# Kernel tuning notes

Hardware: AMD Instinct MI355X
Metric: run time of the kernel (lower is better)

Reference implementation:

```python
import jax, jax.numpy as jnp
import numpy as np

DIM = 512
NUM_HEADS = 8
HEAD_DIM = DIM // NUM_HEADS        # 64
L_HEADS = 4                        # int(8 * 0.5)
H_HEADS = NUM_HEADS - L_HEADS      # 4
L_DIM = L_HEADS * HEAD_DIM         # 256
H_DIM = H_HEADS * HEAD_DIM         # 256
WS = 2                             # window_size
SCALE = HEAD_DIM ** -0.5
SEQ_LEN = 1024


def setup_inputs() -> dict:
    key = jax.random.key(0)
    ks = jax.random.split(key, 13)
    B, N, C = 16, 1024, DIM
    def w(k, shape, fan_in):
        return (jax.random.normal(k, shape, jnp.float32) / np.sqrt(fan_in)).astype(jnp.float32)
    return {
        "x": jax.random.normal(ks[0], (B, N, C), jnp.float32),
        "pos_emb": jax.random.normal(ks[1], (1, SEQ_LEN, C), jnp.float32) * 0.02,
        "l_q_w": w(ks[2], (C, L_DIM), C),
        "l_kv_w": w(ks[3], (C, 2 * L_DIM), C),
        "l_proj_w": w(ks[4], (L_DIM, L_DIM), L_DIM),
        "l_proj_b": jax.random.normal(ks[5], (L_DIM,), jnp.float32) * 0.01,
        "h_qkv_w": w(ks[6], (C, 3 * H_DIM), C),
        "h_proj_w": w(ks[7], (H_DIM, H_DIM), H_DIM),
        "h_proj_b": jax.random.normal(ks[8], (H_DIM,), jnp.float32) * 0.01,
        "in_proj_w": w(ks[9], (C, 3 * C), C),
        "in_proj_b": jax.random.normal(ks[10], (3 * C,), jnp.float32) * 0.01,
        "out_proj_w": w(ks[11], (C, C), C),
        "out_proj_b": jax.random.normal(ks[12], (C,), jnp.float32) * 0.01,
        "H": 32,
        "W": 32,
    }


def _hifi(xg, h_qkv_w, h_proj_w, h_proj_b, H, W):
    B, _, _, C = xg.shape
    hg, wg = H // WS, W // WS
    G, T = hg * wg, WS * WS
    # [B, hg, WS, wg, WS, C] -> [B, G, T, C] (window partition)
    xw = xg.reshape(B, hg, WS, wg, WS, C).transpose(0, 1, 3, 2, 4, 5).reshape(B, G, T, C)
    qkv = (xw @ h_qkv_w).reshape(B, G, T, 3, H_HEADS, HEAD_DIM)
    q = qkv[:, :, :, 0].transpose(0, 1, 3, 2, 4)  # [B,G,h,T,d]
    k = qkv[:, :, :, 1].transpose(0, 1, 3, 2, 4)
    v = qkv[:, :, :, 2].transpose(0, 1, 3, 2, 4)
    attn = jax.nn.softmax(jnp.einsum("bghtd,bghsd->bghts", q, k) * SCALE, axis=-1)
    o = jnp.einsum("bghts,bghsd->bghtd", attn, v)
    # window un-partition: [B,G,h,T,d] -> [B,H,W,h_dim]
    o = o.transpose(0, 1, 3, 2, 4).reshape(B, hg, wg, WS, WS, H_DIM)
    o = o.transpose(0, 1, 3, 2, 4, 5).reshape(B, H, W, H_DIM)
    return o @ h_proj_w + h_proj_b


def _lofi(xg, l_q_w, l_kv_w, l_proj_w, l_proj_b, H, W):
    B, _, _, C = xg.shape
    N = H * W
    q = (xg @ l_q_w).reshape(B, N, L_HEADS, HEAD_DIM)
    kv = (xg @ l_kv_w).reshape(B, N, 2, L_HEADS, HEAD_DIM)
    k, v = kv[:, :, 0], kv[:, :, 1]
    attn = jax.nn.softmax(jnp.einsum("bnhd,bmhd->bhnm", q, k) * SCALE, axis=-1)
    o = jnp.einsum("bhnm,bmhd->bnhd", attn, v).reshape(B, H, W, L_DIM)
    return o @ l_proj_w + l_proj_b


def _mha(y, in_proj_w, in_proj_b, out_proj_w, out_proj_b):
    B, N, C = y.shape
    qkv = y @ in_proj_w + in_proj_b
    q, k, v = jnp.split(qkv, 3, axis=-1)
    q = q.reshape(B, N, NUM_HEADS, HEAD_DIM)
    k = k.reshape(B, N, NUM_HEADS, HEAD_DIM)
    v = v.reshape(B, N, NUM_HEADS, HEAD_DIM)
    attn = jax.nn.softmax(jnp.einsum("bnhd,bmhd->bhnm", q, k) * SCALE, axis=-1)
    o = jnp.einsum("bhnm,bmhd->bnhd", attn, v).reshape(B, N, C)
    return o @ out_proj_w + out_proj_b


def reference(x, pos_emb, l_q_w, l_kv_w, l_proj_w, l_proj_b,
              h_qkv_w, h_proj_w, h_proj_b,
              in_proj_w, in_proj_b, out_proj_w, out_proj_b, H, W):
    B, N, C = x.shape
    x = x + pos_emb[:, :N, :]
    xg = x.reshape(B, H, W, C)
    hifi_out = _hifi(xg, h_qkv_w, h_proj_w, h_proj_b, H, W)
    lofi_out = _lofi(xg, l_q_w, l_kv_w, l_proj_w, l_proj_b, H, W)
    y = jnp.concatenate([hifi_out, lofi_out], axis=-1).reshape(B, N, C)
    return _mha(y, in_proj_w, in_proj_b, out_proj_w, out_proj_b)
```

## Files before the change

### kernel.cpp

```cpp
#include <hip/hip_runtime.h>

typedef unsigned short ushort_t;
typedef short bf16x8 __attribute__((ext_vector_type(8)));
typedef float f32x4 __attribute__((ext_vector_type(4)));
typedef float f32x16 __attribute__((ext_vector_type(16)));

#define DEV __device__ __forceinline__

DEV ushort_t f2bf(float f) {
  return (ushort_t)((__float_as_uint(f) + 0x8000u) >> 16);
}
DEV unsigned pk_bf16(float lo, float hi) {
  unsigned a = __float_as_uint(lo) + 0x8000u;
  unsigned b = __float_as_uint(hi) + 0x8000u;
  return __builtin_amdgcn_perm(b, a, 0x07060302);
}
DEV float bf2f(ushort_t h) {
  union { unsigned int u; float f; } v; v.u = ((unsigned int)h) << 16;
  return v.f;
}
DEV f32x4 mfma16(bf16x8 a, bf16x8 b, f32x4 c) {
  return __builtin_amdgcn_mfma_f32_16x16x32_bf16(a, b, c, 0, 0, 0);
}
DEV f32x16 mfma32(bf16x8 a, bf16x8 b, f32x16 c) {
  return __builtin_amdgcn_mfma_f32_32x32x16_bf16(a, b, c, 0, 0, 0);
}
DEV void pl32swap(unsigned &a, unsigned &b) {
  asm("v_permlane32_swap_b32 %0, %1" : "+v"(a), "+v"(b));
}
typedef __attribute__((address_space(3))) void lds_void;
typedef const __attribute__((address_space(1))) void glb_void;
DEV void gl_lds16(const void* g, void* l) {
  __builtin_amdgcn_global_load_lds((glb_void*)g, (lds_void*)l, 16, 0, 0);
}

__global__ __launch_bounds__(256)
void gemm_bt(const ushort_t* __restrict__ A, int lda,
             const ushort_t* __restrict__ BT,
             const float* __restrict__ bias,
             ushort_t* __restrict__ Cb, float* __restrict__ Cf,
             int ldc, int coff, int K, float scv, int sc_lo, int sc_hi)
{
  __shared__ __align__(16) ushort_t As[128 * 32];
  __shared__ __align__(16) ushort_t Bs[128 * 32];
  const int tid  = threadIdx.x;
  const int wave = tid >> 6, lane = tid & 63;
  const int quad = lane >> 4, r16 = lane & 15;
  const int m0 = blockIdx.x * 128, n0 = blockIdx.y * 128;
  const int wm = (wave >> 1) * 64, wn = (wave & 1) * 64;

  f32x4 acc[4][4];
#pragma unroll
  for (int i = 0; i < 4; ++i)
#pragma unroll
    for (int j = 0; j < 4; ++j) acc[i][j] = (f32x4){0.f, 0.f, 0.f, 0.f};

  for (int kc = 0; kc < K; kc += 32) {
#pragma unroll
    for (int p = 0; p < 4; ++p) {
      int wp = p * 4 + wave;
      int lc = ((wp & 7) << 6) + lane;
      int row = lc >> 2, e8 = (lc & 3) * 8;
      if (wp < 8) gl_lds16(&A[(size_t)(m0 + row) * lda + kc + e8], &As[lc * 8]);
      else        gl_lds16(&BT[(size_t)(n0 + row) * K  + kc + e8], &Bs[lc * 8]);
    }
    __syncthreads();
    bf16x8 af[4], bfr[4];
#pragma unroll
    for (int i = 0; i < 4; ++i) {
      af[i]  = *(const bf16x8*)&As[(wm + i * 16 + r16) * 32 + quad * 8];
      bfr[i] = *(const bf16x8*)&Bs[(wn + i * 16 + r16) * 32 + quad * 8];
    }
#pragma unroll
    for (int mi = 0; mi < 4; ++mi)
#pragma unroll
      for (int ni = 0; ni < 4; ++ni)
        acc[mi][ni] = mfma16(af[mi], bfr[ni], acc[mi][ni]);
    __syncthreads();
  }

#pragma unroll
  for (int mi = 0; mi < 4; ++mi) {
#pragma unroll
    for (int ni = 0; ni < 4; ++ni) {
      int col = n0 + wn + ni * 16 + r16;
      float bv = bias ? bias[col] : 0.f;
      float s = (col >= sc_lo && col < sc_hi) ? scv : 1.0f;
#pragma unroll
      for (int r = 0; r < 4; ++r) {
        int row = m0 + wm + mi * 16 + quad * 4 + r;
        float v = (acc[mi][ni][r] + bv) * s;
        if (Cf) Cf[(size_t)row * ldc + coff + col] = v;
        else    Cb[(size_t)row * ldc + coff + col] = f2bf(v);
      }
    }
  }
}

template<int QG>
__global__ __launch_bounds__(256, 2)
void flash_attn9(const ushort_t* __restrict__ Q, int qs, int q_ch,
                 const ushort_t* __restrict__ Kg, int ks, int k_ch,
                 const ushort_t* __restrict__ vT,
                 ushort_t* __restrict__ O, int os, int o_ch,
                 int N)
{
  __shared__ __align__(16) ushort_t Ks[2][64 * 64];
  __shared__ __align__(16) ushort_t Vs[2][64 * 64];

  const int H = gridDim.y;
  const int tid = threadIdx.x, wave = tid >> 6, lane = tid & 63;
  const int c = lane & 31, hh = lane >> 5;

  const int nwg = gridDim.x * H * gridDim.z;
  const int lin = blockIdx.x + gridDim.x * (blockIdx.y + H * blockIdx.z);
  const int logical = (lin & 7) * (nwg >> 3) + (lin >> 3);
  const int QBS = 8 / QG;
  const int qb = logical & (QBS - 1);
  const int t8 = logical / QBS;
  const int b = (H == 8) ? (t8 >> 3) : (t8 >> 2);
  const int h = t8 - b * H;
  const int q0 = qb * (128 * QG) + wave * (32 * QG);

  bf16x8 qf[QG][4];
#pragma unroll
  for (int qg = 0; qg < QG; ++qg) {
    const ushort_t* qp =
        Q + ((size_t)b * N + q0 + qg * 32 + c) * qs + q_ch + h * 64 + hh * 8;
#pragma unroll
    for (int s = 0; s < 4; ++s) qf[qg][s] = *(const bf16x8*)&qp[s * 16];
  }
  const ushort_t* kbase = Kg + ((size_t)b * N) * ks + k_ch + h * 64;
  const ushort_t* vbase = vT + ((size_t)(b * H + h) * 64) * N;

  f32x16 oacc[QG][2];
#pragma unroll
  for (int qg = 0; qg < QG; ++qg)
#pragma unroll
    for (int i = 0; i < 16; ++i) { oacc[qg][0][i] = 0.f; oacc[qg][1][i] = 0.f; }
  float l_acc[QG];
#pragma unroll
  for (int qg = 0; qg < QG; ++qg) l_acc[qg] = 0.f;

  auto stage = [&](int s0, int buf) {
#pragma unroll
    for (int p = 0; p < 4; ++p) {
      int wp = p * 4 + wave;
      int lc = ((wp & 7) << 6) + lane;
      int row = lc >> 3, cc = lc & 7;
      int e8 = ((cc ^ (row & 7)) * 8);
      if (wp < 8) gl_lds16(kbase + (size_t)(s0 + row) * ks + e8, &Ks[buf][lc * 8]);
      else        gl_lds16(vbase + (size_t)row * N + s0 + e8,    &Vs[buf][lc * 8]);
    }
  };

  stage(0, 0);
  const int NT = N >> 6;
  for (int it = 0; it < NT; ++it) {
    const int cur = it & 1;
    __syncthreads();
    if (it + 1 < NT) stage((it + 1) << 6, cur ^ 1);

    bf16x8 Bf[QG][4];
#pragma unroll
    for (int kb = 0; kb < 2; ++kb) {
      const int krow = kb * 32 + c;
      const ushort_t* kr = &Ks[cur][krow * 64];
      bf16x8 kf[4];
#pragma unroll
      for (int s = 0; s < 4; ++s)
        kf[s] = *(const bf16x8*)&kr[(((s << 1) + hh) ^ (krow & 7)) * 8];

#pragma unroll
      for (int qg = 0; qg < QG; ++qg) {
        f32x16 z;
#pragma unroll
        for (int i = 0; i < 16; ++i) z[i] = 0.f;
#pragma unroll
        for (int s = 0; s < 4; ++s) z = mfma32(kf[s], qf[qg][s], z);
        float ts = 0.f;
        unsigned W[8];
#pragma unroll
        for (int t = 0; t < 8; ++t) {
          float p0 = __builtin_amdgcn_exp2f(z[2 * t]);
          float p1 = __builtin_amdgcn_exp2f(z[2 * t + 1]);
          ts += p0 + p1;
          W[t] = pk_bf16(p0, p1);
        }
        l_acc[qg] += ts;
        union U8 { bf16x8 f; unsigned u[4]; } f0, f1;
        unsigned a0 = W[0], b0 = W[2]; pl32swap(a0, b0);
        unsigned a1 = W[1], b1 = W[3]; pl32swap(a1, b1);
        f0.u[0] = a0; f0.u[1] = a1; f0.u[2] = b0; f0.u[3] = b1;
        unsigned a2 = W[4], b2 = W[6]; pl32swap(a2, b2);
        unsigned a3 = W[5], b3 = W[7]; pl32swap(a3, b3);
        f1.u[0] = a2; f1.u[1] = a3; f1.u[2] = b2; f1.u[3] = b3;
        Bf[qg][kb * 2]     = f0.f;
        Bf[qg][kb * 2 + 1] = f1.f;
      }
    }

#pragma unroll
    for (int db = 0; db < 2; ++db) {
      const int vrow = db * 32 + c;
      const ushort_t* vr = &Vs[cur][vrow * 64];
      bf16x8 vf[4];
#pragma unroll
      for (int s = 0; s < 4; ++s)
        vf[s] = *(const bf16x8*)&vr[(((s << 1) + hh) ^ (vrow & 7)) * 8];
#pragma unroll
      for (int qg = 0; qg < QG; ++qg)
#pragma unroll
        for (int s = 0; s < 4; ++s)
          oacc[qg][db] = mfma32(vf[s], Bf[qg][s], oacc[qg][db]);
    }
  }

#pragma unroll
  for (int qg = 0; qg < QG; ++qg) {
    float l = l_acc[qg] + __shfl_xor(l_acc[qg], 32);
    float inv = 1.f / l;
    ushort_t* op = O + ((size_t)b * N + q0 + qg * 32 + c) * os + o_ch + h * 64;
#pragma unroll
    for (int db = 0; db < 2; ++db) {
#pragma unroll
      for (int g = 0; g < 4; ++g) {
        uint2 pkv;
        pkv.x = pk_bf16(oacc[qg][db][4 * g + 0] * inv, oacc[qg][db][4 * g + 1] * inv);
        pkv.y = pk_bf16(oacc[qg][db][4 * g + 2] * inv, oacc[qg][db][4 * g + 3] * inv);
        *(uint2*)&op[db * 32 + g * 8 + hh * 4] = pkv;
      }
    }
  }
}

__global__ __launch_bounds__(256)
void transpose_v(const ushort_t* __restrict__ in, int ld, int ch,
                 ushort_t* __restrict__ out, int N, int H)
{
  __shared__ __align__(16) ushort_t T[64][72];
  const int s0 = blockIdx.x * 64, h = blockIdx.y, b = blockIdx.z;
  const int tid = threadIdx.x;
#pragma unroll
  for (int p = 0; p < 2; ++p) {
    int c = p * 256 + tid;
    int sr = c >> 3, d0 = (c & 7) * 8;
    *(uint4*)&T[sr][d0] =
        *(const uint4*)&in[((size_t)b * N + s0 + sr) * ld + ch + h * 64 + d0];
  }
  __syncthreads();
  const int d = tid >> 2, sp = (tid & 3) * 16;
  union { uint4 v; ushort_t u[8]; } A, B;
#pragma unroll
  for (int j = 0; j < 8; ++j) { A.u[j] = T[sp + j][d]; B.u[j] = T[sp + 8 + j][d]; }
  ushort_t* op = out + ((size_t)(b * H + h) * 64 + d) * N + s0 + sp;
  *(uint4*)&op[0] = A.v;
  *(uint4*)&op[8] = B.v;
}

__global__ __launch_bounds__(256)
void hifi_win(const ushort_t* __restrict__ qkv, int ld, ushort_t* __restrict__ out)
{
  const int bg = blockIdx.x;
  const int b = bg >> 8, g = bg & 255;
  const int head = threadIdx.x >> 6, lane = threadIdx.x & 63;
  const int gh = g >> 4, gw = g & 15;

  int n[4];
  float q[4], k[4], v[4];
#pragma unroll
  for (int t = 0; t < 4; ++t) {
    n[t] = (gh * 2 + (t >> 1)) * 32 + gw * 2 + (t & 1);
    size_t base = ((size_t)b * 1024 + n[t]) * ld + head * 64 + lane;
    q[t] = bf2f(qkv[base]);
    k[t] = bf2f(qkv[base + 256]);
    v[t] = bf2f(qkv[base + 512]);
  }
  float sc[4][4];
#pragma unroll
  for (int t = 0; t < 4; ++t)
#pragma unroll
    for (int s = 0; s < 4; ++s) {
      float p = q[t] * k[s];
#pragma unroll
      for (int off = 32; off >= 1; off >>= 1) p += __shfl_xor(p, off);
      sc[t][s] = p * 0.125f;
    }
#pragma unroll
  for (int t = 0; t < 4; ++t) {
    float m = fmaxf(fmaxf(sc[t][0], sc[t][1]), fmaxf(sc[t][2], sc[t][3]));
    float p0 = __expf(sc[t][0] - m), p1 = __expf(sc[t][1] - m);
    float p2 = __expf(sc[t][2] - m), p3 = __expf(sc[t][3] - m);
    float sum = p0 + p1 + p2 + p3;
    float o = (p0 * v[0] + p1 * v[1] + p2 * v[2] + p3 * v[3]) / sum;
    out[((size_t)b * 1024 + n[t]) * 512 + head * 64 + lane] = f2bf(o);
  }
}

struct WEnt { const float* W; ushort_t* WT; int K; int N; };
struct WArgs { WEnt e[7]; };

__global__ __launch_bounds__(256)
void w_prep(WArgs a)
{
  WEnt w = a.e[blockIdx.z];
  if ((int)blockIdx.x >= (w.K >> 6) || (int)blockIdx.y >= (w.N >> 6)) return;
  __shared__ float T[64][65];
  const int k0 = blockIdx.x * 64, n0 = blockIdx.y * 64;
  const int tid = threadIdx.x;
#pragma unroll
  for (int p = 0; p < 4; ++p) {
    int c = p * 256 + tid;
    int kr = c >> 4, f4 = (c & 15) * 4;
    float4 v = *(const float4*)&w.W[(size_t)(k0 + kr) * w.N + n0 + f4];
    T[f4 + 0][kr] = v.x; T[f4 + 1][kr] = v.y;
    T[f4 + 2][kr] = v.z; T[f4 + 3][kr] = v.w;
  }
  __syncthreads();
  const int nl = tid >> 2, kp = (tid & 3) * 16;
  union { uint4 v; ushort_t u[8]; } A, B;
#pragma unroll
  for (int j = 0; j < 8; ++j) {
    A.u[j] = f2bf(T[nl][kp + j]);
    B.u[j] = f2bf(T[nl][kp + 8 + j]);
  }
  ushort_t* op = w.WT + (size_t)(n0 + nl) * w.K + k0 + kp;
  *(uint4*)&op[0] = A.v;
  *(uint4*)&op[8] = B.v;
}

__global__ void add_pos(const float* __restrict__ x, const float* __restrict__ pos,
                        ushort_t* __restrict__ xpe)
{
  int idx = blockIdx.x * 256 + threadIdx.x;
  int e = idx * 4;
  float4 xv = *(const float4*)&x[e];
  float4 pv = *(const float4*)&pos[e & (512 * 1024 - 1)];
  uint2 pk;
  pk.x = pk_bf16(xv.x + pv.x, xv.y + pv.y);
  pk.y = pk_bf16(xv.z + pv.z, xv.w + pv.w);
  *(uint2*)&xpe[e] = pk;
}

extern "C" void kernel_launch(void* const* d_in, const int* in_sizes, int n_in,
                              void* d_out, int out_size, void* d_ws, size_t ws_size,
                              hipStream_t stream)
{
  const float* x         = (const float*)d_in[0];
  const float* pos       = (const float*)d_in[1];
  const float* l_q_w     = (const float*)d_in[2];
  const float* l_kv_w    = (const float*)d_in[3];
  const float* l_proj_w  = (const float*)d_in[4];
  const float* l_proj_b  = (const float*)d_in[5];
  const float* h_qkv_w   = (const float*)d_in[6];
  const float* h_proj_w  = (const float*)d_in[7];
  const float* h_proj_b  = (const float*)d_in[8];
  const float* in_proj_w = (const float*)d_in[9];
  const float* in_proj_b = (const float*)d_in[10];
  const float* out_proj_w= (const float*)d_in[11];
  const float* out_proj_b= (const float*)d_in[12];
  float* out = (float*)d_out;

  const float QSCALE = 0.125f * 1.44269504f;

  char* ws = (char*)d_ws;
  ushort_t* xpe = (ushort_t*)(ws);
  ushort_t* y   = (ushort_t*)(ws + (size_t)16777216);
  ushort_t* F   = (ushort_t*)(ws + (size_t)33554432);
  ushort_t* rB  = (ushort_t*)(ws + (size_t)83886080);
  ushort_t* wb  = (ushort_t*)(ws + (size_t)100663296);

  ushort_t* F_T      = wb;
  ushort_t* h_projT  = wb + 786432;
  ushort_t* l_projT  = wb + 851968;
  ushort_t* in_projT = wb + 917504;
  ushort_t* out_projT= wb + 1703936;

  const int M = 16384;
  ushort_t* vT_lo = xpe;
  ushort_t* vT_m  = rB;

  WArgs wa;
  wa.e[0] = {h_qkv_w,   F_T,                 512, 768};
  wa.e[1] = {l_q_w,     F_T + 768 * 512,     512, 256};
  wa.e[2] = {l_kv_w,    F_T + 1024 * 512,    512, 512};
  wa.e[3] = {h_proj_w,  h_projT,             256, 256};
  wa.e[4] = {l_proj_w,  l_projT,             256, 256};
  wa.e[5] = {in_proj_w, in_projT,            512, 1536};
  wa.e[6] = {out_proj_w,out_projT,           512, 512};
  w_prep<<<dim3(8, 24, 7), dim3(256), 0, stream>>>(wa);

  add_pos<<<dim3(8192), dim3(256), 0, stream>>>(x, pos, xpe);

  gemm_bt<<<dim3(M / 128, 12), dim3(256), 0, stream>>>(
      xpe, 512, F_T, nullptr, F, nullptr, 1536, 0, 512, QSCALE, 768, 1024);
  hifi_win<<<dim3(4096), dim3(256), 0, stream>>>(F, 1536, rB);
  transpose_v<<<dim3(16, 4, 16), dim3(256), 0, stream>>>(
      F, 1536, 1280, vT_lo, 1024, 4);
  flash_attn9<1><<<dim3(8, 4, 16), dim3(256), 0, stream>>>(
      F, 1536, 768, F, 1536, 1024, vT_lo, rB, 512, 256, 1024);
  gemm_bt<<<dim3(M / 128, 2), dim3(256), 0, stream>>>(
      rB, 512, h_projT, h_proj_b, y, nullptr, 512, 0, 256, 1.0f, 0, 0);
  gemm_bt<<<dim3(M / 128, 2), dim3(256), 0, stream>>>(
      rB + 256, 512, l_projT, l_proj_b, y, nullptr, 512, 256, 256, 1.0f, 0, 0);
  gemm_bt<<<dim3(M / 128, 12), dim3(256), 0, stream>>>(
      y, 512, in_projT, in_proj_b, F, nullptr, 1536, 0, 512, QSCALE, 0, 512);
  transpose_v<<<dim3(16, 8, 16), dim3(256), 0, stream>>>(
      F, 1536, 1024, vT_m, 1024, 8);
  flash_attn9<2><<<dim3(4, 8, 16), dim3(256), 0, stream>>>(
      F, 1536, 0, F, 1536, 512, vT_m, xpe, 512, 0, 1024);
  gemm_bt<<<dim3(M / 128, 4), dim3(256), 0, stream>>>(
      xpe, 512, out_projT, out_proj_b, nullptr, out, 512, 0, 512, 1.0f, 0, 0);
}
```

Before: 335.4 us.

## Merge hifi/lofi projection GEMMs, remap GEMM tiles across XCDs, use hardware bf16 pack

```diff
diff --git a/kernel.cpp b/kernel.cpp
--- a/kernel.cpp
+++ b/kernel.cpp
@@ -14,6 +14,11 @@
   unsigned a = __float_as_uint(lo) + 0x8000u;
   unsigned b = __float_as_uint(hi) + 0x8000u;
   return __builtin_amdgcn_perm(b, a, 0x07060302);
+}
+DEV unsigned cvtpk_bf16(float lo, float hi) {
+  unsigned r;
+  asm("v_cvt_pk_bf16_f32 %0, %1, %2" : "=v"(r) : "v"(lo), "v"(hi));
+  return r;
 }
 DEV float bf2f(ushort_t h) {
   union { unsigned int u; float f; } v; v.u = ((unsigned int)h) << 16;
@@ -46,7 +51,12 @@
   const int tid  = threadIdx.x;
   const int wave = tid >> 6, lane = tid & 63;
   const int quad = lane >> 4, r16 = lane & 15;
-  const int m0 = blockIdx.x * 128, n0 = blockIdx.y * 128;
+  const int nwg = gridDim.x * gridDim.y;
+  const int lin = blockIdx.x + gridDim.x * blockIdx.y;
+  const int logical = (lin & 7) * (nwg >> 3) + (lin >> 3);
+  const int nbn = gridDim.y;
+  const int mb = logical / nbn, nb = logical - mb * nbn;
+  const int m0 = mb * 128, n0 = nb * 128;
   const int wm = (wave >> 1) * 64, wn = (wave & 1) * 64;
 
   f32x4 acc[4][4];
@@ -92,6 +102,72 @@
         float v = (acc[mi][ni][r] + bv) * s;
         if (Cf) Cf[(size_t)row * ldc + coff + col] = v;
         else    Cb[(size_t)row * ldc + coff + col] = f2bf(v);
+      }
+    }
+  }
+}
+
+__global__ __launch_bounds__(256)
+void gemm_proj(const ushort_t* __restrict__ rB,
+               const ushort_t* __restrict__ hT, const ushort_t* __restrict__ lT,
+               const float* __restrict__ hb, const float* __restrict__ lb,
+               ushort_t* __restrict__ y)
+{
+  __shared__ __align__(16) ushort_t As[128 * 32];
+  __shared__ __align__(16) ushort_t Bs[128 * 32];
+  const int tid  = threadIdx.x;
+  const int wave = tid >> 6, lane = tid & 63;
+  const int quad = lane >> 4, r16 = lane & 15;
+  const int lin = blockIdx.x + 128 * blockIdx.y;
+  const int logical = (lin & 7) * 64 + (lin >> 3);
+  const int nidx = logical & 3, m0 = (logical >> 2) * 128;
+  const int sel = nidx >> 1, n0 = (nidx & 1) * 128;
+  const ushort_t* A  = rB + sel * 256;
+  const ushort_t* BT = sel ? lT : hT;
+  const float* bias  = sel ? lb : hb;
+  const int coff = sel * 256;
+  const int wm = (wave >> 1) * 64, wn = (wave & 1) * 64;
+
+  f32x4 acc[4][4];
+#pragma unroll
+  for (int i = 0; i < 4; ++i)
+#pragma unroll
+    for (int j = 0; j < 4; ++j) acc[i][j] = (f32x4){0.f, 0.f, 0.f, 0.f};
+
+  for (int kc = 0; kc < 256; kc += 32) {
+#pragma unroll
+    for (int p = 0; p < 4; ++p) {
+      int wp = p * 4 + wave;
+      int lc = ((wp & 7) << 6) + lane;
+      int row = lc >> 2, e8 = (lc & 3) * 8;
+      if (wp < 8) gl_lds16(&A[(size_t)(m0 + row) * 512 + kc + e8], &As[lc * 8]);
+      else        gl_lds16(&BT[(size_t)(n0 + row) * 256 + kc + e8], &Bs[lc * 8]);
+    }
+    __syncthreads();
+    bf16x8 af[4], bfr[4];
+#pragma unroll
+    for (int i = 0; i < 4; ++i) {
+      af[i]  = *(const bf16x8*)&As[(wm + i * 16 + r16) * 32 + quad * 8];
+      bfr[i] = *(const bf16x8*)&Bs[(wn + i * 16 + r16) * 32 + quad * 8];
+    }
+#pragma unroll
+    for (int mi = 0; mi < 4; ++mi)
+#pragma unroll
+      for (int ni = 0; ni < 4; ++ni)
+        acc[mi][ni] = mfma16(af[mi], bfr[ni], acc[mi][ni]);
+    __syncthreads();
+  }
+
+#pragma unroll
+  for (int mi = 0; mi < 4; ++mi) {
+#pragma unroll
+    for (int ni = 0; ni < 4; ++ni) {
+      int col = n0 + wn + ni * 16 + r16;
+      float bv = bias[col];
+#pragma unroll
+      for (int r = 0; r < 4; ++r) {
+        int row = m0 + wm + mi * 16 + quad * 4 + r;
+        y[(size_t)row * 512 + coff + col] = f2bf(acc[mi][ni][r] + bv);
       }
     }
   }
@@ -185,7 +261,7 @@
           float p0 = __builtin_amdgcn_exp2f(z[2 * t]);
           float p1 = __builtin_amdgcn_exp2f(z[2 * t + 1]);
           ts += p0 + p1;
-          W[t] = pk_bf16(p0, p1);
+          W[t] = cvtpk_bf16(p0, p1);
         }
         l_acc[qg] += ts;
         union U8 { bf16x8 f; unsigned u[4]; } f0, f1;
@@ -226,8 +302,8 @@
 #pragma unroll
       for (int g = 0; g < 4; ++g) {
         uint2 pkv;
-        pkv.x = pk_bf16(oacc[qg][db][4 * g + 0] * inv, oacc[qg][db][4 * g + 1] * inv);
-        pkv.y = pk_bf16(oacc[qg][db][4 * g + 2] * inv, oacc[qg][db][4 * g + 3] * inv);
+        pkv.x = cvtpk_bf16(oacc[qg][db][4 * g + 0] * inv, oacc[qg][db][4 * g + 1] * inv);
+        pkv.y = cvtpk_bf16(oacc[qg][db][4 * g + 2] * inv, oacc[qg][db][4 * g + 3] * inv);
         *(uint2*)&op[db * 32 + g * 8 + hh * 4] = pkv;
       }
     }
@@ -399,10 +475,8 @@
       F, 1536, 1280, vT_lo, 1024, 4);
   flash_attn9<1><<<dim3(8, 4, 16), dim3(256), 0, stream>>>(
       F, 1536, 768, F, 1536, 1024, vT_lo, rB, 512, 256, 1024);
-  gemm_bt<<<dim3(M / 128, 2), dim3(256), 0, stream>>>(
-      rB, 512, h_projT, h_proj_b, y, nullptr, 512, 0, 256, 1.0f, 0, 0);
-  gemm_bt<<<dim3(M / 128, 2), dim3(256), 0, stream>>>(
-      rB + 256, 512, l_projT, l_proj_b, y, nullptr, 512, 256, 256, 1.0f, 0, 0);
+  gemm_proj<<<dim3(128, 4), dim3(256), 0, stream>>>(
+      rB, h_projT, l_projT, h_proj_b, l_proj_b, y);
   gemm_bt<<<dim3(M / 128, 12), dim3(256), 0, stream>>>(
       y, 512, in_projT, in_proj_b, F, nullptr, 1536, 0, 512, QSCALE, 0, 512);
   transpose_v<<<dim3(16, 8, 16), dim3(256), 0, stream>>>(
```

After: 313.7 us. -6.5%, faster.
